# Kernel optimization log

Measured on AMD Instinct MI355X. Metric: run time of the kernel, lower is better.

Reference implementation:

```python
import jax, jax.numpy as jnp
import numpy as np

D_ENC, D_PRED, D_JOINT, VOCAB = 512, 512, 640, 1024


def setup_inputs() -> dict:
    key = jax.random.key(0)
    k1, k2, k3, k4, k5, k6 = jax.random.split(key, 6)
    B, T, U1 = 8, 256, 64
    enc_out = jax.random.normal(k1, (B, T, D_ENC), dtype=jnp.float32)
    pred_out = jax.random.normal(k2, (B, U1, D_PRED), dtype=jnp.float32)
    # Linear weights, torch convention [out, in]; kaiming-uniform-ish scale
    W_enc = jax.random.normal(k3, (D_JOINT, D_ENC), dtype=jnp.float32) / np.sqrt(D_ENC)
    W_pred = jax.random.normal(k4, (D_JOINT, D_PRED), dtype=jnp.float32) / np.sqrt(D_PRED)
    W_out = jax.random.normal(k5, (VOCAB, D_JOINT), dtype=jnp.float32) / np.sqrt(D_JOINT)
    b_out = jax.random.normal(k6, (VOCAB,), dtype=jnp.float32) * 0.01
    return {"enc_out": enc_out, "pred_out": pred_out, "W_enc": W_enc,
            "W_pred": W_pred, "W_out": W_out, "b_out": b_out}


def reference(enc_out, pred_out, W_enc, W_pred, W_out, b_out):
    # f: [B, T, d_joint], g: [B, U+1, d_joint]
    f = jnp.einsum("btd,jd->btj", enc_out, W_enc)
    g = jnp.einsum("bud,jd->buj", pred_out, W_pred)
    # broadcast add -> [B, T, U+1, d_joint], tanh, project to vocab
    combined = jnp.tanh(f[:, :, None, :] + g[:, None, :, :])
    logits = jnp.einsum("btuj,vj->btuv", combined, W_out) + b_out
    return logits
```

## Files before the change

### kernel.cpp

```cpp
#include <hip/hip_runtime.h>


typedef _Float16 f16x8 __attribute__((ext_vector_type(8)));
typedef float    f32x4 __attribute__((ext_vector_type(4)));

__device__ __forceinline__ float fast_tanh(float x) {
    float e = __builtin_amdgcn_exp2f(x * 2.88539008177792681472f);
    return 1.0f - 2.0f * __builtin_amdgcn_rcpf(e + 1.0f);
}

__device__ __forceinline__ void gll16(const void* g, void* l) {
    __builtin_amdgcn_global_load_lds(
        (const __attribute__((address_space(1))) void*)g,
        (__attribute__((address_space(3))) void*)l, 16, 0, 0);
}

__global__ __launch_bounds__(256) void fg_kernel(
    const float* __restrict__ enc, const float* __restrict__ pred,
    const float* __restrict__ Wenc, const float* __restrict__ Wpred,
    float* __restrict__ fg)
{
    __shared__ float As[64][36];
    __shared__ float WsT[32][68];

    const int bid = blockIdx.x;
    const int mt = bid / 10;
    const int nt = bid % 10;
    const int m0 = mt * 64;
    const int n0 = nt * 64;

    const float* Aptr;
    const float* Wptr;
    if (m0 < 2048) { Aptr = enc  + (size_t)m0 * 512;          Wptr = Wenc; }
    else           { Aptr = pred + (size_t)(m0 - 2048) * 512; Wptr = Wpred; }

    const int t  = threadIdx.x;
    const int ty = t >> 4;
    const int tx = t & 15;
    const int lr = t >> 2;
    const int lc = (t & 3) * 8;
    const int lane6 = t & 63;
    const int w8    = (t >> 6) * 8;

    float acc[4][4];
#pragma unroll
    for (int i = 0; i < 4; ++i)
#pragma unroll
        for (int j = 0; j < 4; ++j) acc[i][j] = 0.0f;

    for (int k0 = 0; k0 < 512; k0 += 32) {
        __syncthreads();
        {
            const float* sa = Aptr + (size_t)lr * 512 + k0 + lc;
            f32x4 a0 = *(const f32x4*)(sa);
            f32x4 a1 = *(const f32x4*)(sa + 4);
            *(f32x4*)&As[lr][lc]     = a0;
            *(f32x4*)&As[lr][lc + 4] = a1;
            const float* sw = Wptr + (size_t)(n0 + lane6) * 512 + k0 + w8;
            f32x4 w0 = *(const f32x4*)(sw);
            f32x4 w1 = *(const f32x4*)(sw + 4);
#pragma unroll
            for (int j = 0; j < 4; ++j) {
                WsT[w8 + j][lane6]     = w0[j];
                WsT[w8 + 4 + j][lane6] = w1[j];
            }
        }
        __syncthreads();
#pragma unroll
        for (int kk = 0; kk < 32; ++kk) {
            float av[4], bv[4];
#pragma unroll
            for (int i = 0; i < 4; ++i) av[i] = As[ty * 4 + i][kk];
#pragma unroll
            for (int j = 0; j < 4; ++j) bv[j] = WsT[kk][tx * 4 + j];
#pragma unroll
            for (int i = 0; i < 4; ++i)
#pragma unroll
                for (int j = 0; j < 4; ++j)
                    acc[i][j] = fmaf(av[i], bv[j], acc[i][j]);
        }
    }

#pragma unroll
    for (int i = 0; i < 4; ++i) {
        f32x4 v = { acc[i][0], acc[i][1], acc[i][2], acc[i][3] };
        *(f32x4*)&fg[(size_t)(m0 + ty * 4 + i) * 640 + n0 + tx * 4] = v;
    }
}

__global__ __launch_bounds__(256) void wconv_kernel(
    const float* __restrict__ W, _Float16* __restrict__ Wh)
{
    const int tid = blockIdx.x * 256 + threadIdx.x;
    const int n   = tid / 80;
    const int c   = tid % 80;
    f32x4 a = *(const f32x4*)(W + (size_t)n * 640 + c * 8);
    f32x4 b = *(const f32x4*)(W + (size_t)n * 640 + c * 8 + 4);
    f16x8 h;
#pragma unroll
    for (int j = 0; j < 4; ++j) { h[j] = (_Float16)a[j]; h[4 + j] = (_Float16)b[j]; }
    const int seg = n >> 4;
    const int kc  = c >> 2;
    const int L   = (n & 15) + 16 * (c & 3);
    *(f16x8*)(Wh + (size_t)seg * 10240 + kc * 512 + L * 8) = h;
}

__global__ __launch_bounds__(256, 2) void joint_kernel(
    const float* __restrict__ fg, const _Float16* __restrict__ Wh,
    const float* __restrict__ bias, float* __restrict__ out)
{
    __shared__ _Float16 Ash0[4 * 528];
    __shared__ _Float16 Ash1[4 * 528];
    __shared__ _Float16 Bsh0[512 * 32];
    __shared__ _Float16 Bsh1[512 * 32];

    const int bid = blockIdx.x;
    const int pp  = bid >> 1;
    const int mt  = (pp & 7) * 256 + (pp >> 3);
    const int nt  = bid & 1;
    const int m0  = mt << 6;
    const int n0s = nt * 32;

    const int t    = threadIdx.x;
    const int lane = t & 63;
    const int wid  = t >> 6;
    const int wn   = wid;
    const int lr   = lane & 15;
    const int lk   = lane >> 4;

    const int r  = t >> 2;
    const int q  = t & 3;
    const int m  = m0 + r;
    const float* grow = fg + (size_t)(2048 + ((m >> 14) << 6) + (m & 63)) * 640;
    const float* frow = fg + (size_t)mt * 640;

    int aoff[4];
#pragma unroll
    for (int mf = 0; mf < 4; ++mf)
        aoff[mf] = lk * 528 + (mf * 16 + lr) * 8;
    int boff[8];
#pragma unroll
    for (int nf = 0; nf < 8; ++nf)
        boff[nf] = (wn * 8 + nf) * 512 + lane * 8;
    const int awoff = q * 528 + r * 8;

    const _Float16* gbase = Wh + (size_t)(n0s + wid * 8) * 10240 + lane * 8;
    int gdst[8];
#pragma unroll
    for (int i = 0; i < 8; ++i)
        gdst[i] = (wid * 8 + i) * 512;

    f32x4 acc[4][8];
#pragma unroll
    for (int i = 0; i < 4; ++i)
#pragma unroll
        for (int j = 0; j < 8; ++j) acc[i][j] = (f32x4){0.f, 0.f, 0.f, 0.f};

    {
        f32x4 fv0 = *(const f32x4*)(frow + q * 8);
        f32x4 fv1 = *(const f32x4*)(frow + q * 8 + 4);
        f32x4 gv0 = *(const f32x4*)(grow + q * 8);
        f32x4 gv1 = *(const f32x4*)(grow + q * 8 + 4);
#pragma unroll
        for (int i = 0; i < 8; ++i)
            gll16(gbase + (size_t)i * 10240, &Bsh0[gdst[i]]);
        f16x8 h;
#pragma unroll
        for (int j = 0; j < 4; ++j) {
            h[j]     = (_Float16)fast_tanh(fv0[j] + gv0[j]);
            h[4 + j] = (_Float16)fast_tanh(fv1[j] + gv1[j]);
        }
        *(f16x8*)&Ash0[awoff] = h;
        __syncthreads();
    }

#define JITER_FULL(K0, CA, CB, NA, NB)                                         \
    {                                                                          \
        const int kn_ = (K0) + 32;                                             \
             \
        f32x4 fv0_ = *(const f32x4*)(frow + kn_ + q * 8);                      \
        f32x4 fv1_ = *(const f32x4*)(frow + kn_ + q * 8 + 4);                  \
        f32x4 gv0_ = *(const f32x4*)(grow + kn_ + q * 8);                      \
        f32x4 gv1_ = *(const f32x4*)(grow + kn_ + q * 8 + 4);                  \
        _Pragma("unroll")                                                      \
        for (int i = 0; i < 8; ++i)                                            \
            gll16(gbase + (size_t)i * 10240 + kn_ * 16, &NB[gdst[i]]);         \
        f16x8 af[4], bf[8];                                                    \
        _Pragma("unroll")                                                      \
        for (int mf = 0; mf < 4; ++mf)                                         \
            af[mf] = *(const f16x8*)&CA[aoff[mf]];                             \
        _Pragma("unroll")                                                      \
        for (int nf = 0; nf < 8; ++nf)                                         \
            bf[nf] = *(const f16x8*)&CB[boff[nf]];                             \
        f16x8 h_;                                                              \
        _Pragma("unroll")                                                      \
        for (int j = 0; j < 4; ++j) {                                          \
            h_[j]     = (_Float16)fast_tanh(fv0_[j] + gv0_[j]);                \
            h_[4 + j] = (_Float16)fast_tanh(fv1_[j] + gv1_[j]);                \
        }                                                                      \
        __builtin_amdgcn_s_setprio(1);                                         \
        _Pragma("unroll")                                                      \
        for (int mf = 0; mf < 4; ++mf)                                         \
            _Pragma("unroll")                                                  \
            for (int nf = 0; nf < 8; ++nf)                                     \
                acc[mf][nf] = __builtin_amdgcn_mfma_f32_16x16x32_f16(          \
                    af[mf], bf[nf], acc[mf][nf], 0, 0, 0);                     \
        __builtin_amdgcn_s_setprio(0);                                         \
        *(f16x8*)&NA[awoff] = h_;                                              \
        __syncthreads();                                                       \
    }

#define JITER_LAST(CA, CB)                                                     \
    {                                                                          \
        f16x8 af[4], bf[8];                                                    \
        _Pragma("unroll")                                                      \
        for (int mf = 0; mf < 4; ++mf)                                         \
            af[mf] = *(const f16x8*)&CA[aoff[mf]];                             \
        _Pragma("unroll")                                                      \
        for (int nf = 0; nf < 8; ++nf)                                         \
            bf[nf] = *(const f16x8*)&CB[boff[nf]];                             \
        __builtin_amdgcn_s_setprio(1);                                         \
        _Pragma("unroll")                                                      \
        for (int mf = 0; mf < 4; ++mf)                                         \
            _Pragma("unroll")                                                  \
            for (int nf = 0; nf < 8; ++nf)                                     \
                acc[mf][nf] = __builtin_amdgcn_mfma_f32_16x16x32_f16(          \
                    af[mf], bf[nf], acc[mf][nf], 0, 0, 0);                     \
        __builtin_amdgcn_s_setprio(0);                                         \
    }

    for (int kc = 0; kc < 18; kc += 2) {
        JITER_FULL(kc * 32,      Ash0, Bsh0, Ash1, Bsh1);
        JITER_FULL(kc * 32 + 32, Ash1, Bsh1, Ash0, Bsh0);
    }
    JITER_FULL(576, Ash0, Bsh0, Ash1, Bsh1);
    JITER_LAST(Ash1, Bsh1);

#undef JITER_FULL
#undef JITER_LAST

    float bv[8];
#pragma unroll
    for (int nf = 0; nf < 8; ++nf)
        bv[nf] = bias[nt * 512 + wn * 128 + nf * 16 + lr];

#pragma unroll
    for (int mf = 0; mf < 4; ++mf) {
#pragma unroll
        for (int rr = 0; rr < 4; ++rr) {
            const int row = m0 + mf * 16 + lk * 4 + rr;
            float* orow = out + (size_t)row * 1024 + nt * 512 + wn * 128;
#pragma unroll
            for (int nf = 0; nf < 8; ++nf)
                orow[nf * 16 + lr] = acc[mf][nf][rr] + bv[nf];
        }
    }
}

extern "C" void kernel_launch(void* const* d_in, const int* in_sizes, int n_in,
                              void* d_out, int out_size, void* d_ws, size_t ws_size,
                              hipStream_t stream) {
    const float* enc   = (const float*)d_in[0];
    const float* pred  = (const float*)d_in[1];
    const float* Wenc  = (const float*)d_in[2];
    const float* Wpred = (const float*)d_in[3];
    const float* Wout  = (const float*)d_in[4];
    const float* bout  = (const float*)d_in[5];

    float*     fg = (float*)d_ws;
    _Float16*  Wh = (_Float16*)((char*)d_ws + 2560 * 640 * 4);

    fg_kernel<<<400, 256, 0, stream>>>(enc, pred, Wenc, Wpred, fg);
    wconv_kernel<<<320, 256, 0, stream>>>(Wout, Wh);
    joint_kernel<<<4096, 256, 0, stream>>>(fg, Wh, bout, (float*)d_out);
}
```

Baseline: 306.1 us.

## Merge the two vocab-half blocks into one 512-thread block sharing the A tile

The joint kernel now launches one 512-thread block per 64-row M tile that covers all 1024 vocab columns, where it previously used two 256-thread blocks that each covered half. Only the first 256 threads compute the tanh(f+g) A tile, and all eight waves consume it, so the A-side loads and tanh work are no longer duplicated across the two halves. In exchange, LDS for the B buffers doubles to 128 KB per block, which may limit how many blocks fit on a CU. The extra waves also idle during A staging.

```diff
diff --git a/kernel.cpp b/kernel.cpp
--- a/kernel.cpp
+++ b/kernel.cpp
@@ -105,21 +105,18 @@
     *(f16x8*)(Wh + (size_t)seg * 10240 + kc * 512 + L * 8) = h;
 }
 
-__global__ __launch_bounds__(256, 2) void joint_kernel(
+__global__ __launch_bounds__(512, 2) void joint_kernel(
     const float* __restrict__ fg, const _Float16* __restrict__ Wh,
     const float* __restrict__ bias, float* __restrict__ out)
 {
     __shared__ _Float16 Ash0[4 * 528];
     __shared__ _Float16 Ash1[4 * 528];
-    __shared__ _Float16 Bsh0[512 * 32];
-    __shared__ _Float16 Bsh1[512 * 32];
+    __shared__ _Float16 Bsh0[64 * 512];
+    __shared__ _Float16 Bsh1[64 * 512];
 
     const int bid = blockIdx.x;
-    const int pp  = bid >> 1;
-    const int mt  = (pp & 7) * 256 + (pp >> 3);
-    const int nt  = bid & 1;
+    const int mt  = (bid & 7) * 256 + (bid >> 3);
     const int m0  = mt << 6;
-    const int n0s = nt * 32;
 
     const int t    = threadIdx.x;
     const int lane = t & 63;
@@ -128,8 +125,9 @@
     const int lr   = lane & 15;
     const int lk   = lane >> 4;
 
-    const int r  = t >> 2;
+    const int r  = (t & 255) >> 2;
     const int q  = t & 3;
+    const bool astage = (t < 256);
     const int m  = m0 + r;
     const float* grow = fg + (size_t)(2048 + ((m >> 14) << 6) + (m & 63)) * 640;
     const float* frow = fg + (size_t)mt * 640;
@@ -144,7 +142,7 @@
         boff[nf] = (wn * 8 + nf) * 512 + lane * 8;
     const int awoff = q * 528 + r * 8;
 
-    const _Float16* gbase = Wh + (size_t)(n0s + wid * 8) * 10240 + lane * 8;
+    const _Float16* gbase = Wh + (size_t)(wid * 8) * 10240 + lane * 8;
     int gdst[8];
 #pragma unroll
     for (int i = 0; i < 8; ++i)
@@ -157,31 +155,36 @@
         for (int j = 0; j < 8; ++j) acc[i][j] = (f32x4){0.f, 0.f, 0.f, 0.f};
 
     {
-        f32x4 fv0 = *(const f32x4*)(frow + q * 8);
-        f32x4 fv1 = *(const f32x4*)(frow + q * 8 + 4);
-        f32x4 gv0 = *(const f32x4*)(grow + q * 8);
-        f32x4 gv1 = *(const f32x4*)(grow + q * 8 + 4);
 #pragma unroll
         for (int i = 0; i < 8; ++i)
             gll16(gbase + (size_t)i * 10240, &Bsh0[gdst[i]]);
-        f16x8 h;
-#pragma unroll
-        for (int j = 0; j < 4; ++j) {
-            h[j]     = (_Float16)fast_tanh(fv0[j] + gv0[j]);
-            h[4 + j] = (_Float16)fast_tanh(fv1[j] + gv1[j]);
-        }
-        *(f16x8*)&Ash0[awoff] = h;
+        if (astage) {
+            f32x4 fv0 = *(const f32x4*)(frow + q * 8);
+            f32x4 fv1 = *(const f32x4*)(frow + q * 8 + 4);
+            f32x4 gv0 = *(const f32x4*)(grow + q * 8);
+            f32x4 gv1 = *(const f32x4*)(grow + q * 8 + 4);
+            f16x8 h;
+#pragma unroll
+            for (int j = 0; j < 4; ++j) {
+                h[j]     = (_Float16)fast_tanh(fv0[j] + gv0[j]);
+                h[4 + j] = (_Float16)fast_tanh(fv1[j] + gv1[j]);
+            }
+            *(f16x8*)&Ash0[awoff] = h;
+        }
         __syncthreads();
     }
 
 #define JITER_FULL(K0, CA, CB, NA, NB)                                         \
     {                                                                          \
         const int kn_ = (K0) + 32;                                             \
-             \
-        f32x4 fv0_ = *(const f32x4*)(frow + kn_ + q * 8);                      \
-        f32x4 fv1_ = *(const f32x4*)(frow + kn_ + q * 8 + 4);                  \
-        f32x4 gv0_ = *(const f32x4*)(grow + kn_ + q * 8);                      \
-        f32x4 gv1_ = *(const f32x4*)(grow + kn_ + q * 8 + 4);                  \
+                \
+        f32x4 fv0_, fv1_, gv0_, gv1_;                                          \
+        if (astage) {                                                          \
+            fv0_ = *(const f32x4*)(frow + kn_ + q * 8);                        \
+            fv1_ = *(const f32x4*)(frow + kn_ + q * 8 + 4);                    \
+            gv0_ = *(const f32x4*)(grow + kn_ + q * 8);                        \
+            gv1_ = *(const f32x4*)(grow + kn_ + q * 8 + 4);                    \
+        }                                                                      \
         _Pragma("unroll")                                                      \
         for (int i = 0; i < 8; ++i)                                            \
             gll16(gbase + (size_t)i * 10240 + kn_ * 16, &NB[gdst[i]]);         \
@@ -193,10 +196,12 @@
         for (int nf = 0; nf < 8; ++nf)                                         \
             bf[nf] = *(const f16x8*)&CB[boff[nf]];                             \
         f16x8 h_;                                                              \
-        _Pragma("unroll")                                                      \
-        for (int j = 0; j < 4; ++j) {                                          \
-            h_[j]     = (_Float16)fast_tanh(fv0_[j] + gv0_[j]);                \
-            h_[4 + j] = (_Float16)fast_tanh(fv1_[j] + gv1_[j]);                \
+        if (astage) {                                                          \
+            _Pragma("unroll")                                                  \
+            for (int j = 0; j < 4; ++j) {                                      \
+                h_[j]     = (_Float16)fast_tanh(fv0_[j] + gv0_[j]);            \
+                h_[4 + j] = (_Float16)fast_tanh(fv1_[j] + gv1_[j]);            \
+            }                                                                  \
         }                                                                      \
         __builtin_amdgcn_s_setprio(1);                                         \
         _Pragma("unroll")                                                      \
@@ -206,7 +211,8 @@
                 acc[mf][nf] = __builtin_amdgcn_mfma_f32_16x16x32_f16(          \
                     af[mf], bf[nf], acc[mf][nf], 0, 0, 0);                     \
         __builtin_amdgcn_s_setprio(0);                                         \
-        *(f16x8*)&NA[awoff] = h_;                                              \
+        if (astage)                                                            \
+            *(f16x8*)&NA[awoff] = h_;                                          \
         __syncthreads();                                                       \
     }
 
@@ -242,14 +248,14 @@
     float bv[8];
 #pragma unroll
     for (int nf = 0; nf < 8; ++nf)
-        bv[nf] = bias[nt * 512 + wn * 128 + nf * 16 + lr];
+        bv[nf] = bias[wn * 128 + nf * 16 + lr];
 
 #pragma unroll
     for (int mf = 0; mf < 4; ++mf) {
 #pragma unroll
         for (int rr = 0; rr < 4; ++rr) {
             const int row = m0 + mf * 16 + lk * 4 + rr;
-            float* orow = out + (size_t)row * 1024 + nt * 512 + wn * 128;
+            float* orow = out + (size_t)row * 1024 + wn * 128;
 #pragma unroll
             for (int nf = 0; nf < 8; ++nf)
                 orow[nf * 16 + lr] = acc[mf][nf][rr] + bv[nf];
@@ -272,5 +278,5 @@
 
     fg_kernel<<<400, 256, 0, stream>>>(enc, pred, Wenc, Wpred, fg);
     wconv_kernel<<<320, 256, 0, stream>>>(Wout, Wh);
-    joint_kernel<<<4096, 256, 0, stream>>>(fg, Wh, bout, (float*)d_out);
-}
+    joint_kernel<<<2048, 512, 0, stream>>>(fg, Wh, bout, (float*)d_out);
+}
```

Result: slower. 318.4 us (+4.0%).
